# Optimization experiments

Hardware: AMD Instinct MI355X
Metric: run time of the kernel (lower is better)

## Reference

```python
import jax, jax.numpy as jnp
import numpy as np

NUM_HOPS = 3
SIGMA = 0.1
EPS = 1e-12  # torch F.normalize default eps


def setup_inputs() -> dict:
    key = jax.random.key(0)
    k1, k2 = jax.random.split(key)
    N, D, E = 50000, 128, 800000
    x = jax.random.normal(k1, (N, D), dtype=jnp.float32)
    edge_index = jax.random.randint(k2, (2, E), 0, N, dtype=jnp.int64)
    return {"x": x, "edge_index": edge_index}


def _l2_normalize(h):
    # matches torch.nn.functional.normalize(x, dim=1)
    n = jnp.linalg.norm(h, axis=1, keepdims=True)
    return h / jnp.maximum(n, EPS)


def reference(x, edge_index):
    N = x.shape[0]
    src, dst = edge_index[0], edge_index[1]
    noise_keys = jax.random.split(jax.random.key(1), NUM_HOPS)

    h = _l2_normalize(x)
    outs = [h]
    for k in range(NUM_HOPS):
        # edge-wise inner-product similarity + sigmoid gate
        e = jnp.sum(h[src] * h[dst], axis=1)          # [E]
        alpha = jax.nn.sigmoid(e)                     # [E]
        # sparse alpha^T @ h == segment-sum over dst of alpha * h[src]
        aggr = jax.ops.segment_sum(alpha[:, None] * h[src], dst, num_segments=N)  # [N, D]
        noised = aggr + SIGMA * jax.random.normal(noise_keys[k], aggr.shape, dtype=x.dtype)
        h = _l2_normalize(noised)
        outs.append(h)
    return jnp.stack(outs)                            # [NUM_HOPS+1, N, D]
```

## Files before the change

### kernel.cpp

```cpp
#include <hip/hip_runtime.h>
#include <cstdint>
#include <cstddef>

#define D 128

__host__ __device__ inline uint32_t rotl32(uint32_t v, int d) {
  return (v << d) | (v >> (32 - d));
}

__host__ __device__ inline void threefry2x32(uint32_t k0, uint32_t k1,
                                             uint32_t x0, uint32_t x1,
                                             uint32_t* o0, uint32_t* o1) {
  uint32_t k2 = k0 ^ k1 ^ 0x1BD11BDAu;
  x0 += k0; x1 += k1;
#define TF_RND(r) x0 += x1; x1 = rotl32(x1, (r)); x1 ^= x0;
  TF_RND(13) TF_RND(15) TF_RND(26) TF_RND(6)
  x0 += k1; x1 += k2 + 1u;
  TF_RND(17) TF_RND(29) TF_RND(16) TF_RND(24)
  x0 += k2; x1 += k0 + 2u;
  TF_RND(13) TF_RND(15) TF_RND(26) TF_RND(6)
  x0 += k0; x1 += k1 + 3u;
  TF_RND(17) TF_RND(29) TF_RND(16) TF_RND(24)
  x0 += k1; x1 += k2 + 4u;
  TF_RND(13) TF_RND(15) TF_RND(26) TF_RND(6)
  x0 += k2; x1 += k0 + 5u;
#undef TF_RND
  *o0 = x0; *o1 = x1;
}

__device__ inline float erfinv_f32(float x) {
  float w = -log1pf(-x * x);
  float p;
  if (w < 5.0f) {
    w = w - 2.5f;
    p = 2.81022636e-08f;
    p = fmaf(p, w, 3.43273939e-07f);
    p = fmaf(p, w, -3.5233877e-06f);
    p = fmaf(p, w, -4.39150654e-06f);
    p = fmaf(p, w, 0.00021858087f);
    p = fmaf(p, w, -0.00125372503f);
    p = fmaf(p, w, -0.00417768164f);
    p = fmaf(p, w, 0.246640727f);
    p = fmaf(p, w, 1.50140941f);
  } else {
    w = sqrtf(w) - 3.0f;
    p = -0.000200214257f;
    p = fmaf(p, w, 0.000100950558f);
    p = fmaf(p, w, 0.00134934322f);
    p = fmaf(p, w, -0.00367342844f);
    p = fmaf(p, w, 0.00573950773f);
    p = fmaf(p, w, -0.0076224613f);
    p = fmaf(p, w, 0.00943887047f);
    p = fmaf(p, w, 1.00167406f);
    p = fmaf(p, w, 2.83297682f);
  }
  return p * x;
}

__device__ inline float jax_normal_elem(uint32_t k0, uint32_t k1, uint32_t idx) {
  uint32_t o0, o1;
  threefry2x32(k0, k1, 0u, idx, &o0, &o1);
  uint32_t bits = o0 ^ o1;
  float f = __uint_as_float((bits >> 9) | 0x3F800000u) - 1.0f;
  float u = f * 2.0f + (-0.99999994f);
  u = fmaxf(-0.99999994f, u);
  return 1.41421356237309505f * erfinv_f32(u);
}

__device__ inline uint32_t f32_to_bf16_rne(float f) {
  uint32_t u = __float_as_uint(f);
  u += 0x7fffu + ((u >> 16) & 1u);
  return u >> 16;
}

__global__ __launch_bounds__(256) void hist4_kernel(
    const int* __restrict__ dst, int* __restrict__ counts, int E4, int E) {
  int t = blockIdx.x * blockDim.x + threadIdx.x;
  if (t < E4) {
    int4 d = ((const int4*)dst)[t];
    atomicAdd(&counts[d.x], 1);
    atomicAdd(&counts[d.y], 1);
    atomicAdd(&counts[d.z], 1);
    atomicAdd(&counts[d.w], 1);
  }
  int rem = E4 * 4 + t;
  if (t < E - E4 * 4) atomicAdd(&counts[dst[rem]], 1);
}

__global__ __launch_bounds__(256) void scanA_kernel(
    int* __restrict__ counts, int* __restrict__ blocksums, int N) {
  __shared__ int tmp[256];
  int tid = threadIdx.x;
  int i = blockIdx.x * 256 + tid;
  int v = (i < N) ? counts[i] : 0;
  tmp[tid] = v;
  __syncthreads();
  for (int off = 1; off < 256; off <<= 1) {
    int t = (tid >= off) ? tmp[tid - off] : 0;
    __syncthreads();
    tmp[tid] += t;
    __syncthreads();
  }
  if (i < N) counts[i] = tmp[tid] - v;
  if (tid == 255) blocksums[blockIdx.x] = tmp[tid];
}

__global__ __launch_bounds__(256) void scanB_kernel(
    int* __restrict__ blocksums, int nb) {
  __shared__ int tmp[256];
  int tid = threadIdx.x;
  int v = (tid < nb) ? blocksums[tid] : 0;
  tmp[tid] = v;
  __syncthreads();
  for (int off = 1; off < 256; off <<= 1) {
    int t = (tid >= off) ? tmp[tid - off] : 0;
    __syncthreads();
    tmp[tid] += t;
    __syncthreads();
  }
  if (tid < nb) blocksums[tid] = tmp[tid] - v;
}

__global__ __launch_bounds__(256) void scanC_kernel(
    int* __restrict__ offsets, int* __restrict__ cursor,
    const int* __restrict__ blocksums, int N, int E) {
  int i = blockIdx.x * 256 + threadIdx.x;
  if (i < N) {
    int o = offsets[i] + blocksums[blockIdx.x];
    offsets[i] = o;
    cursor[i] = o;
  }
  if (i == 0) offsets[N] = E;
}

__global__ __launch_bounds__(256) void deghist_kernel(
    const int* __restrict__ offsets, int* __restrict__ deg_hist, int N) {
  __shared__ int lhist[1024];
  for (int b = threadIdx.x; b < 1024; b += 256) lhist[b] = 0;
  __syncthreads();
  int i = blockIdx.x * 256 + threadIdx.x;
  if (i < N) {
    int d = min(offsets[i + 1] - offsets[i], 1023);
    atomicAdd(&lhist[d], 1);
  }
  __syncthreads();
  for (int b = threadIdx.x; b < 1024; b += 256) {
    int c = lhist[b];
    if (c) atomicAdd(&deg_hist[b], c);
  }
}

__global__ __launch_bounds__(256) void degscan_kernel(
    const int* __restrict__ deg_hist, int* __restrict__ deg_cursor) {
  __shared__ int tmp[256];
  int tid = threadIdx.x;
  int loc[4], s = 0;
#pragma unroll
  for (int k = 0; k < 4; ++k) { loc[k] = deg_hist[tid * 4 + k]; s += loc[k]; }
  tmp[tid] = s;
  __syncthreads();
  for (int off = 1; off < 256; off <<= 1) {
    int t = (tid >= off) ? tmp[tid - off] : 0;
    __syncthreads();
    tmp[tid] += t;
    __syncthreads();
  }
  int run = tmp[tid] - s;
#pragma unroll
  for (int k = 0; k < 4; ++k) { deg_cursor[tid * 4 + k] = run; run += loc[k]; }
}

__global__ __launch_bounds__(256) void degscatter_kernel(
    const int* __restrict__ offsets, int* __restrict__ deg_cursor,
    int* __restrict__ perm, int N) {
  __shared__ int lhist[1024];
  __shared__ int lbase[1024];
  for (int b = threadIdx.x; b < 1024; b += 256) lhist[b] = 0;
  __syncthreads();
  int i = blockIdx.x * 256 + threadIdx.x;
  int d = 0, lpos = 0;
  if (i < N) {
    d = min(offsets[i + 1] - offsets[i], 1023);
    lpos = atomicAdd(&lhist[d], 1);
  }
  __syncthreads();
  for (int b = threadIdx.x; b < 1024; b += 256) {
    int c = lhist[b];
    lbase[b] = c ? atomicAdd(&deg_cursor[b], c) : 0;
  }
  __syncthreads();
  if (i < N) perm[lbase[d] + lpos] = i;
}

__global__ __launch_bounds__(256) void edgescatter4_kernel(
    const int* __restrict__ src, const int* __restrict__ dst,
    int* __restrict__ cursor, int* __restrict__ sorted_src, int E4, int E) {
  int t = blockIdx.x * blockDim.x + threadIdx.x;
  if (t < E4) {
    int4 d = ((const int4*)dst)[t];
    int4 s = ((const int4*)src)[t];
    sorted_src[atomicAdd(&cursor[d.x], 1)] = s.x;
    sorted_src[atomicAdd(&cursor[d.y], 1)] = s.y;
    sorted_src[atomicAdd(&cursor[d.z], 1)] = s.z;
    sorted_src[atomicAdd(&cursor[d.w], 1)] = s.w;
  }
  int rem = E4 * 4 + t;
  if (t < E - E4 * 4) {
    int d = dst[rem];
    sorted_src[atomicAdd(&cursor[d], 1)] = src[rem];
  }
}

__global__ __launch_bounds__(256) void norm_kernel(
    const float* __restrict__ in, float* __restrict__ out,
    uint16_t* __restrict__ mir, int N) {
  int t = blockIdx.x * blockDim.x + threadIdx.x;
  int row = t >> 6;
  int lane = t & 63;
  if (row >= N) return;
  size_t base = (size_t)row * D + 2 * lane;
  float2 v = *(const float2*)(in + base);
  float ss = v.x * v.x + v.y * v.y;
#pragma unroll
  for (int off = 32; off > 0; off >>= 1) ss += __shfl_xor(ss, off);
  float denom = fmaxf(sqrtf(ss), 1e-12f);
  float2 o = make_float2(v.x / denom, v.y / denom);
  *(float2*)(out + base) = o;
  if (mir) {
    uint32_t w = f32_to_bf16_rne(o.x) | (f32_to_bf16_rne(o.y) << 16);
    *(uint32_t*)(mir + base) = w;
  }
}

union V8 { float4 v[2]; float f[8]; };
union U4B { uint4 v; uint32_t u[4]; };

__device__ inline void cvt8(const U4B& a, V8& af) {
#pragma unroll
  for (int i = 0; i < 4; ++i) {
    af.f[2 * i] = __uint_as_float(a.u[i] << 16);
    af.f[2 * i + 1] = __uint_as_float(a.u[i] & 0xffff0000u);
  }
}

__global__ __launch_bounds__(256) void hop_kernel_bf16(
    const float* __restrict__ hprev, const uint16_t* __restrict__ mprev,
    float* __restrict__ hout, uint16_t* __restrict__ mout,
    const int* __restrict__ offsets, const int* __restrict__ sorted_src,
    const int* __restrict__ perm, int N, int E, uint32_t k0, uint32_t k1) {
  int g = (blockIdx.x * blockDim.x + threadIdx.x) >> 4;
  int sub = threadIdx.x & 15;
  if (g >= N) return;
  int r = perm[g];
  size_t rbase = (size_t)r * D + sub * 8;

  V8 b;
  {
    const float4* p = (const float4*)(hprev + rbase);
    b.v[0] = p[0]; b.v[1] = p[1];
  }
  V8 acc;
#pragma unroll
  for (int i = 0; i < 8; ++i) acc.f[i] = 0.f;

  int j0 = offsets[r];
  int cnt = offsets[r + 1] - j0;
  int Em1 = E - 1;

  int s1 = sorted_src[min(j0 + 1, Em1)];
  int s2 = sorted_src[min(j0 + 2, Em1)];
  int s3 = sorted_src[min(j0 + 3, Em1)];
  U4B a0, a1, a2;
  {
    int s0 = sorted_src[min(j0, Em1)];
    a0.v = *(const uint4*)(mprev + (size_t)s0 * D + sub * 8);
  }
  a1.v = *(const uint4*)(mprev + (size_t)s1 * D + sub * 8);
  a2.v = *(const uint4*)(mprev + (size_t)s2 * D + sub * 8);

  for (int i = 0; i < cnt; ++i) {
    int s4 = sorted_src[min(j0 + i + 4, Em1)];
    U4B a3;
    a3.v = *(const uint4*)(mprev + (size_t)s3 * D + sub * 8);

    V8 af;
    cvt8(a0, af);
    float part = af.f[0] * b.f[0];
#pragma unroll
    for (int q = 1; q < 8; ++q) part = fmaf(af.f[q], b.f[q], part);
    part += __shfl_xor(part, 1);
    part += __shfl_xor(part, 2);
    part += __shfl_xor(part, 4);
    part += __shfl_xor(part, 8);
    float alpha = __builtin_amdgcn_rcpf(1.0f + __expf(-part));
#pragma unroll
    for (int q = 0; q < 8; ++q) acc.f[q] = fmaf(alpha, af.f[q], acc.f[q]);

    a0 = a1; a1 = a2; a2 = a3;
    s3 = s4;
  }

  uint32_t idx = (uint32_t)rbase;
  float ss = 0.f;
#pragma unroll
  for (int i = 0; i < 8; ++i) {
    acc.f[i] += 0.1f * jax_normal_elem(k0, k1, idx + (uint32_t)i);
    ss = fmaf(acc.f[i], acc.f[i], ss);
  }
  ss += __shfl_xor(ss, 1);
  ss += __shfl_xor(ss, 2);
  ss += __shfl_xor(ss, 4);
  ss += __shfl_xor(ss, 8);
  float denom = fmaxf(sqrtf(ss), 1e-12f);
#pragma unroll
  for (int i = 0; i < 8; ++i) acc.f[i] = acc.f[i] / denom;
  {
    float4* p = (float4*)(hout + rbase);
    p[0] = acc.v[0]; p[1] = acc.v[1];
  }
  if (mout) {
    U4B w;
#pragma unroll
    for (int i = 0; i < 4; ++i)
      w.u[i] = f32_to_bf16_rne(acc.f[2 * i]) |
               (f32_to_bf16_rne(acc.f[2 * i + 1]) << 16);
    *(uint4*)(mout + rbase) = w.v;
  }
}

union V16 { float4 v[4]; float f[16]; };

__global__ __launch_bounds__(256) void hop_kernel_f32(
    const float* __restrict__ hprev, float* __restrict__ hout,
    const int* __restrict__ offsets, const int* __restrict__ sorted_src,
    const int* __restrict__ perm, int N, uint32_t k0, uint32_t k1) {
  int g = (blockIdx.x * blockDim.x + threadIdx.x) >> 3;
  int sub = threadIdx.x & 7;
  if (g >= N) return;
  int r = perm[g];
  size_t rbase = (size_t)r * D + sub * 16;

  V16 b;
  {
    const float4* p = (const float4*)(hprev + rbase);
    b.v[0] = p[0]; b.v[1] = p[1]; b.v[2] = p[2]; b.v[3] = p[3];
  }
  V16 acc;
#pragma unroll
  for (int i = 0; i < 16; ++i) acc.f[i] = 0.f;

  int j = offsets[r], jhi = offsets[r + 1];
  V16 a;
  if (j < jhi) {
    const float4* p = (const float4*)(hprev + (size_t)sorted_src[j] * D + sub * 16);
    a.v[0] = p[0]; a.v[1] = p[1]; a.v[2] = p[2]; a.v[3] = p[3];
  }
  while (j < jhi) {
    int jn = j + 1;
    V16 an;
    if (jn < jhi) {
      const float4* p = (const float4*)(hprev + (size_t)sorted_src[jn] * D + sub * 16);
      an.v[0] = p[0]; an.v[1] = p[1]; an.v[2] = p[2]; an.v[3] = p[3];
    }
    float part = a.f[0] * b.f[0];
#pragma unroll
    for (int i = 1; i < 16; ++i) part = fmaf(a.f[i], b.f[i], part);
    part += __shfl_xor(part, 1);
    part += __shfl_xor(part, 2);
    part += __shfl_xor(part, 4);
    float alpha = 1.0f / (1.0f + expf(-part));
#pragma unroll
    for (int i = 0; i < 16; ++i) acc.f[i] = fmaf(alpha, a.f[i], acc.f[i]);
    a = an;
    j = jn;
  }

  uint32_t idx = (uint32_t)rbase;
  float ss = 0.f;
#pragma unroll
  for (int i = 0; i < 16; ++i) {
    acc.f[i] += 0.1f * jax_normal_elem(k0, k1, idx + (uint32_t)i);
    ss = fmaf(acc.f[i], acc.f[i], ss);
  }
  ss += __shfl_xor(ss, 1);
  ss += __shfl_xor(ss, 2);
  ss += __shfl_xor(ss, 4);
  float denom = fmaxf(sqrtf(ss), 1e-12f);
#pragma unroll
  for (int i = 0; i < 16; ++i) acc.f[i] = acc.f[i] / denom;
  {
    float4* p = (float4*)(hout + rbase);
    p[0] = acc.v[0]; p[1] = acc.v[1]; p[2] = acc.v[2]; p[3] = acc.v[3];
  }
}

extern "C" void kernel_launch(void* const* d_in, const int* in_sizes, int n_in,
                              void* d_out, int out_size, void* d_ws, size_t ws_size,
                              hipStream_t stream) {
  const float* x = (const float*)d_in[0];
  const int* ei = (const int*)d_in[1];
  int N = in_sizes[0] / D;
  int E = in_sizes[1] / 2;
  const int* src = ei;
  const int* dst = ei + E;
  float* out = (float*)d_out;
  size_t ND = (size_t)N * D;

  int nblocksN = (N + 255) / 256;

  int* offsets = (int*)d_ws;
  int* cursor = offsets + (N + 1);
  int* perm = cursor + N;
  int* deg_hist = perm + N;
  int* deg_cursor = deg_hist + 1024;
  int* blocksums = deg_cursor + 1024;
  int* sorted_src = blocksums + 256;
  size_t intWords = (size_t)(N + 1) + N + N + 1024 + 1024 + 256 + E;
  size_t mirOff = (intWords * 4 + 255) & ~(size_t)255;
  size_t need = mirOff + 2 * ND * sizeof(uint16_t);
  bool use_bf16 = ws_size >= need;
  uint16_t* mir0 = (uint16_t*)((char*)d_ws + mirOff);
  uint16_t* mir1 = mir0 + ND;

  uint32_t nk0[3], nk1[3];
  for (int k = 0; k < 3; ++k)
    threefry2x32(0u, 1u, 0u, (uint32_t)k, &nk0[k], &nk1[k]);

  int E4 = E / 4;
  int e4Blocks = (max(E4, E - E4 * 4) + 255) / 256;
  int rowWaveBlocks = (int)(((size_t)N * 64 + 255) / 256);
  int hopBlocks16 = (int)(((size_t)N * 16 + 255) / 256);
  int hopBlocks8 = (int)(((size_t)N * 8 + 255) / 256);

  hipMemsetAsync(offsets, 0, (size_t)(N + 1) * sizeof(int), stream);
  hipMemsetAsync(deg_hist, 0, 1024 * sizeof(int), stream);
  hipLaunchKernelGGL(hist4_kernel, dim3(e4Blocks), dim3(256), 0, stream,
                     dst, offsets, E4, E);
  hipLaunchKernelGGL(scanA_kernel, dim3(nblocksN), dim3(256), 0, stream,
                     offsets, blocksums, N);
  hipLaunchKernelGGL(scanB_kernel, dim3(1), dim3(256), 0, stream, blocksums, nblocksN);
  hipLaunchKernelGGL(scanC_kernel, dim3(nblocksN), dim3(256), 0, stream,
                     offsets, cursor, blocksums, N, E);
  hipLaunchKernelGGL(deghist_kernel, dim3(nblocksN), dim3(256), 0, stream,
                     offsets, deg_hist, N);
  hipLaunchKernelGGL(degscan_kernel, dim3(1), dim3(256), 0, stream,
                     deg_hist, deg_cursor);
  hipLaunchKernelGGL(degscatter_kernel, dim3(nblocksN), dim3(256), 0, stream,
                     offsets, deg_cursor, perm, N);
  hipLaunchKernelGGL(edgescatter4_kernel, dim3(e4Blocks), dim3(256), 0, stream,
                     src, dst, cursor, sorted_src, E4, E);

  hipLaunchKernelGGL(norm_kernel, dim3(rowWaveBlocks), dim3(256), 0, stream,
                     x, out, use_bf16 ? mir0 : (uint16_t*)nullptr, N);

  if (use_bf16) {
    uint16_t* mirs[4] = {mir0, mir1, mir0, nullptr};
    for (int k = 0; k < 3; ++k) {
      const float* hk = out + (size_t)k * ND;
      float* hk1 = out + (size_t)(k + 1) * ND;
      hipLaunchKernelGGL(hop_kernel_bf16, dim3(hopBlocks16), dim3(256), 0, stream,
                         hk, mirs[k], hk1, mirs[k + 1], offsets, sorted_src,
                         perm, N, E, nk0[k], nk1[k]);
    }
  } else {
    for (int k = 0; k < 3; ++k) {
      const float* hk = out + (size_t)k * ND;
      float* hk1 = out + (size_t)(k + 1) * ND;
      hipLaunchKernelGGL(hop_kernel_f32, dim3(hopBlocks8), dim3(256), 0, stream,
                         hk, hk1, offsets, sorted_src, perm, N, nk0[k], nk1[k]);
    }
  }
}
```

Baseline: 405.4 us.

## Fold degree-sort kernels into CSR scan and deepen gather prefetch in hop kernel

Merges the degree histogram, degree scan and degree scatter into the existing scanA/scanB/scanC kernels, so three launches and one memset go away. Degrees are cached in a new workspace array instead of being recomputed from offsets. The bf16 hop kernel now keeps a 4-deep ring buffer of gathered neighbor rows and sets a launch-bounds occupancy hint, which raises memory-level parallelism at some register cost. The fused scanA adds a 1024-entry shared histogram per block, and the workspace grows by N ints.

Measured after the change: 386.9 us. -4.6%, faster.

```diff
diff --git a/kernel.cpp b/kernel.cpp
--- a/kernel.cpp
+++ b/kernel.cpp
@@ -74,7 +74,11 @@
 }
 
 __global__ __launch_bounds__(256) void hist4_kernel(
-    const int* __restrict__ dst, int* __restrict__ counts, int E4, int E) {
+    const int* __restrict__ dst, int* __restrict__ counts,
+    int* __restrict__ deg_hist, int E4, int E) {
+  if (blockIdx.x == 0) {
+    for (int b = threadIdx.x; b < 1024; b += 256) deg_hist[b] = 0;
+  }
   int t = blockIdx.x * blockDim.x + threadIdx.x;
   if (t < E4) {
     int4 d = ((const int4*)dst)[t];
@@ -88,13 +92,20 @@
 }
 
 __global__ __launch_bounds__(256) void scanA_kernel(
-    int* __restrict__ counts, int* __restrict__ blocksums, int N) {
+    int* __restrict__ counts, int* __restrict__ blocksums,
+    int* __restrict__ deg, int* __restrict__ deg_hist, int N) {
   __shared__ int tmp[256];
+  __shared__ int lhist[1024];
+  for (int b = threadIdx.x; b < 1024; b += 256) lhist[b] = 0;
   int tid = threadIdx.x;
   int i = blockIdx.x * 256 + tid;
   int v = (i < N) ? counts[i] : 0;
   tmp[tid] = v;
   __syncthreads();
+  if (i < N) {
+    deg[i] = v;
+    atomicAdd(&lhist[min(v, 1023)], 1);
+  }
   for (int off = 1; off < 256; off <<= 1) {
     int t = (tid >= off) ? tmp[tid - off] : 0;
     __syncthreads();
@@ -103,10 +114,16 @@
   }
   if (i < N) counts[i] = tmp[tid] - v;
   if (tid == 255) blocksums[blockIdx.x] = tmp[tid];
+  __syncthreads();
+  for (int b = threadIdx.x; b < 1024; b += 256) {
+    int c = lhist[b];
+    if (c) atomicAdd(&deg_hist[b], c);
+  }
 }
 
 __global__ __launch_bounds__(256) void scanB_kernel(
-    int* __restrict__ blocksums, int nb) {
+    int* __restrict__ blocksums, int nb,
+    const int* __restrict__ deg_hist, int* __restrict__ deg_cursor) {
   __shared__ int tmp[256];
   int tid = threadIdx.x;
   int v = (tid < nb) ? blocksums[tid] : 0;
@@ -119,70 +136,42 @@
     __syncthreads();
   }
   if (tid < nb) blocksums[tid] = tmp[tid] - v;
+  __syncthreads();
+  int loc[4], s = 0;
+#pragma unroll
+  for (int k = 0; k < 4; ++k) { loc[k] = deg_hist[tid * 4 + k]; s += loc[k]; }
+  __syncthreads();
+  tmp[tid] = s;
+  __syncthreads();
+  for (int off = 1; off < 256; off <<= 1) {
+    int t = (tid >= off) ? tmp[tid - off] : 0;
+    __syncthreads();
+    tmp[tid] += t;
+    __syncthreads();
+  }
+  int run = tmp[tid] - s;
+#pragma unroll
+  for (int k = 0; k < 4; ++k) { deg_cursor[tid * 4 + k] = run; run += loc[k]; }
 }
 
 __global__ __launch_bounds__(256) void scanC_kernel(
     int* __restrict__ offsets, int* __restrict__ cursor,
-    const int* __restrict__ blocksums, int N, int E) {
+    const int* __restrict__ blocksums, const int* __restrict__ deg,
+    int* __restrict__ deg_cursor, int* __restrict__ perm, int N, int E) {
+  __shared__ int lhist[1024];
+  __shared__ int lbase[1024];
+  for (int b = threadIdx.x; b < 1024; b += 256) lhist[b] = 0;
+  __syncthreads();
   int i = blockIdx.x * 256 + threadIdx.x;
+  int d = 0, lpos = 0;
   if (i < N) {
     int o = offsets[i] + blocksums[blockIdx.x];
     offsets[i] = o;
     cursor[i] = o;
+    d = min(deg[i], 1023);
+    lpos = atomicAdd(&lhist[d], 1);
   }
   if (i == 0) offsets[N] = E;
-}
-
-__global__ __launch_bounds__(256) void deghist_kernel(
-    const int* __restrict__ offsets, int* __restrict__ deg_hist, int N) {
-  __shared__ int lhist[1024];
-  for (int b = threadIdx.x; b < 1024; b += 256) lhist[b] = 0;
-  __syncthreads();
-  int i = blockIdx.x * 256 + threadIdx.x;
-  if (i < N) {
-    int d = min(offsets[i + 1] - offsets[i], 1023);
-    atomicAdd(&lhist[d], 1);
-  }
-  __syncthreads();
-  for (int b = threadIdx.x; b < 1024; b += 256) {
-    int c = lhist[b];
-    if (c) atomicAdd(&deg_hist[b], c);
-  }
-}
-
-__global__ __launch_bounds__(256) void degscan_kernel(
-    const int* __restrict__ deg_hist, int* __restrict__ deg_cursor) {
-  __shared__ int tmp[256];
-  int tid = threadIdx.x;
-  int loc[4], s = 0;
-#pragma unroll
-  for (int k = 0; k < 4; ++k) { loc[k] = deg_hist[tid * 4 + k]; s += loc[k]; }
-  tmp[tid] = s;
-  __syncthreads();
-  for (int off = 1; off < 256; off <<= 1) {
-    int t = (tid >= off) ? tmp[tid - off] : 0;
-    __syncthreads();
-    tmp[tid] += t;
-    __syncthreads();
-  }
-  int run = tmp[tid] - s;
-#pragma unroll
-  for (int k = 0; k < 4; ++k) { deg_cursor[tid * 4 + k] = run; run += loc[k]; }
-}
-
-__global__ __launch_bounds__(256) void degscatter_kernel(
-    const int* __restrict__ offsets, int* __restrict__ deg_cursor,
-    int* __restrict__ perm, int N) {
-  __shared__ int lhist[1024];
-  __shared__ int lbase[1024];
-  for (int b = threadIdx.x; b < 1024; b += 256) lhist[b] = 0;
-  __syncthreads();
-  int i = blockIdx.x * 256 + threadIdx.x;
-  int d = 0, lpos = 0;
-  if (i < N) {
-    d = min(offsets[i + 1] - offsets[i], 1023);
-    lpos = atomicAdd(&lhist[d], 1);
-  }
   __syncthreads();
   for (int b = threadIdx.x; b < 1024; b += 256) {
     int c = lhist[b];
@@ -235,15 +224,26 @@
 union V8 { float4 v[2]; float f[8]; };
 union U4B { uint4 v; uint32_t u[4]; };
 
-__device__ inline void cvt8(const U4B& a, V8& af) {
+__device__ inline void hop_edge(const U4B& raw, const V8& b, V8& acc) {
+  V8 af;
 #pragma unroll
   for (int i = 0; i < 4; ++i) {
-    af.f[2 * i] = __uint_as_float(a.u[i] << 16);
-    af.f[2 * i + 1] = __uint_as_float(a.u[i] & 0xffff0000u);
-  }
-}
-
-__global__ __launch_bounds__(256) void hop_kernel_bf16(
+    af.f[2 * i] = __uint_as_float(raw.u[i] << 16);
+    af.f[2 * i + 1] = __uint_as_float(raw.u[i] & 0xffff0000u);
+  }
+  float part = af.f[0] * b.f[0];
+#pragma unroll
+  for (int q = 1; q < 8; ++q) part = fmaf(af.f[q], b.f[q], part);
+  part += __shfl_xor(part, 1);
+  part += __shfl_xor(part, 2);
+  part += __shfl_xor(part, 4);
+  part += __shfl_xor(part, 8);
+  float alpha = __builtin_amdgcn_rcpf(1.0f + __expf(-part));
+#pragma unroll
+  for (int q = 0; q < 8; ++q) acc.f[q] = fmaf(alpha, af.f[q], acc.f[q]);
+}
+
+__global__ __launch_bounds__(256, 4) void hop_kernel_bf16(
     const float* __restrict__ hprev, const uint16_t* __restrict__ mprev,
     float* __restrict__ hout, uint16_t* __restrict__ mout,
     const int* __restrict__ offsets, const int* __restrict__ sorted_src,
@@ -266,46 +266,39 @@
   int j0 = offsets[r];
   int cnt = offsets[r + 1] - j0;
   int Em1 = E - 1;
-
-  int s1 = sorted_src[min(j0 + 1, Em1)];
-  int s2 = sorted_src[min(j0 + 2, Em1)];
-  int s3 = sorted_src[min(j0 + 3, Em1)];
-  U4B a0, a1, a2;
-  {
-    int s0 = sorted_src[min(j0, Em1)];
-    a0.v = *(const uint4*)(mprev + (size_t)s0 * D + sub * 8);
-  }
-  a1.v = *(const uint4*)(mprev + (size_t)s1 * D + sub * 8);
-  a2.v = *(const uint4*)(mprev + (size_t)s2 * D + sub * 8);
-
-  for (int i = 0; i < cnt; ++i) {
-    int s4 = sorted_src[min(j0 + i + 4, Em1)];
-    U4B a3;
-    a3.v = *(const uint4*)(mprev + (size_t)s3 * D + sub * 8);
-
-    V8 af;
-    cvt8(a0, af);
-    float part = af.f[0] * b.f[0];
-#pragma unroll
-    for (int q = 1; q < 8; ++q) part = fmaf(af.f[q], b.f[q], part);
-    part += __shfl_xor(part, 1);
-    part += __shfl_xor(part, 2);
-    part += __shfl_xor(part, 4);
-    part += __shfl_xor(part, 8);
-    float alpha = __builtin_amdgcn_rcpf(1.0f + __expf(-part));
-#pragma unroll
-    for (int q = 0; q < 8; ++q) acc.f[q] = fmaf(alpha, af.f[q], acc.f[q]);
-
-    a0 = a1; a1 = a2; a2 = a3;
-    s3 = s4;
-  }
+  const uint16_t* mp = mprev + sub * 8;
+
+  U4B buf[4];
+  int sNext[4];
+#pragma unroll
+  for (int q = 0; q < 4; ++q) {
+    int s = sorted_src[min(j0 + q, Em1)];
+    buf[q].v = *(const uint4*)(mp + (size_t)s * D);
+  }
+#pragma unroll
+  for (int q = 0; q < 4; ++q) sNext[q] = sorted_src[min(j0 + 4 + q, Em1)];
+
+  int cnt4 = cnt & ~3;
+  int i = 0;
+  for (; i < cnt4; i += 4) {
+#pragma unroll
+    for (int q = 0; q < 4; ++q) {
+      hop_edge(buf[q], b, acc);
+      buf[q].v = *(const uint4*)(mp + (size_t)sNext[q] * D);
+      sNext[q] = sorted_src[min(j0 + i + 8 + q, Em1)];
+    }
+  }
+  int rem = cnt - cnt4;
+#pragma unroll
+  for (int q = 0; q < 3; ++q)
+    if (q < rem) hop_edge(buf[q], b, acc);
 
   uint32_t idx = (uint32_t)rbase;
   float ss = 0.f;
 #pragma unroll
-  for (int i = 0; i < 8; ++i) {
-    acc.f[i] += 0.1f * jax_normal_elem(k0, k1, idx + (uint32_t)i);
-    ss = fmaf(acc.f[i], acc.f[i], ss);
+  for (int i2 = 0; i2 < 8; ++i2) {
+    acc.f[i2] += 0.1f * jax_normal_elem(k0, k1, idx + (uint32_t)i2);
+    ss = fmaf(acc.f[i2], acc.f[i2], ss);
   }
   ss += __shfl_xor(ss, 1);
   ss += __shfl_xor(ss, 2);
@@ -313,7 +306,7 @@
   ss += __shfl_xor(ss, 8);
   float denom = fmaxf(sqrtf(ss), 1e-12f);
 #pragma unroll
-  for (int i = 0; i < 8; ++i) acc.f[i] = acc.f[i] / denom;
+  for (int i2 = 0; i2 < 8; ++i2) acc.f[i2] = acc.f[i2] / denom;
   {
     float4* p = (float4*)(hout + rbase);
     p[0] = acc.v[0]; p[1] = acc.v[1];
@@ -321,9 +314,9 @@
   if (mout) {
     U4B w;
 #pragma unroll
-    for (int i = 0; i < 4; ++i)
-      w.u[i] = f32_to_bf16_rne(acc.f[2 * i]) |
-               (f32_to_bf16_rne(acc.f[2 * i + 1]) << 16);
+    for (int i2 = 0; i2 < 4; ++i2)
+      w.u[i2] = f32_to_bf16_rne(acc.f[2 * i2]) |
+                (f32_to_bf16_rne(acc.f[2 * i2 + 1]) << 16);
     *(uint4*)(mout + rbase) = w.v;
   }
 }
@@ -411,11 +404,12 @@
   int* offsets = (int*)d_ws;
   int* cursor = offsets + (N + 1);
   int* perm = cursor + N;
-  int* deg_hist = perm + N;
+  int* deg = perm + N;
+  int* deg_hist = deg + N;
   int* deg_cursor = deg_hist + 1024;
   int* blocksums = deg_cursor + 1024;
   int* sorted_src = blocksums + 256;
-  size_t intWords = (size_t)(N + 1) + N + N + 1024 + 1024 + 256 + E;
+  size_t intWords = (size_t)(N + 1) + N + N + N + 1024 + 1024 + 256 + E;
   size_t mirOff = (intWords * 4 + 255) & ~(size_t)255;
   size_t need = mirOff + 2 * ND * sizeof(uint16_t);
   bool use_bf16 = ws_size >= need;
@@ -433,20 +427,14 @@
   int hopBlocks8 = (int)(((size_t)N * 8 + 255) / 256);
 
   hipMemsetAsync(offsets, 0, (size_t)(N + 1) * sizeof(int), stream);
-  hipMemsetAsync(deg_hist, 0, 1024 * sizeof(int), stream);
   hipLaunchKernelGGL(hist4_kernel, dim3(e4Blocks), dim3(256), 0, stream,
-                     dst, offsets, E4, E);
+                     dst, offsets, deg_hist, E4, E);
   hipLaunchKernelGGL(scanA_kernel, dim3(nblocksN), dim3(256), 0, stream,
-                     offsets, blocksums, N);
-  hipLaunchKernelGGL(scanB_kernel, dim3(1), dim3(256), 0, stream, blocksums, nblocksN);
+                     offsets, blocksums, deg, deg_hist, N);
+  hipLaunchKernelGGL(scanB_kernel, dim3(1), dim3(256), 0, stream,
+                     blocksums, nblocksN, deg_hist, deg_cursor);
   hipLaunchKernelGGL(scanC_kernel, dim3(nblocksN), dim3(256), 0, stream,
-                     offsets, cursor, blocksums, N, E);
-  hipLaunchKernelGGL(deghist_kernel, dim3(nblocksN), dim3(256), 0, stream,
-                     offsets, deg_hist, N);
-  hipLaunchKernelGGL(degscan_kernel, dim3(1), dim3(256), 0, stream,
-                     deg_hist, deg_cursor);
-  hipLaunchKernelGGL(degscatter_kernel, dim3(nblocksN), dim3(256), 0, stream,
-                     offsets, deg_cursor, perm, N);
+                     offsets, cursor, blocksums, deg, deg_cursor, perm, N, E);
   hipLaunchKernelGGL(edgescatter4_kernel, dim3(e4Blocks), dim3(256), 0, stream,
                      src, dst, cursor, sorted_src, E4, E);
 
```
